# Kernel tuning notes

Hardware: AMD Instinct MI355X
Metric: run time of the kernel (lower is better)

Reference implementation:

```python
import jax, jax.numpy as jnp
import numpy as np

G, T, E, D, C = 4, 2048, 8, 1024, 2048
CAP_FACTORS = (0.25, 0.25, 0.125, 0.125, 0.0625, 0.0625, 0.0625, 0.0625)


def setup_inputs() -> dict:
    key = jax.random.key(0)
    k1, k2 = jax.random.split(key, 2)
    token_inputs = jax.random.normal(k1, (G, T, D), dtype=jnp.float32)
    # RouterWeights: Linear(dim -> num_experts), weight ~ N(0, 0.02), bias = 0
    W = jax.random.normal(k2, (E, D), dtype=jnp.float32) * 0.02
    b = jnp.zeros((E,), dtype=jnp.float32)
    return {"token_inputs": token_inputs, "W": W, "b": b,
            "num_experts": E, "expert_capacity": C}


def reference(token_inputs, W, b, num_experts, expert_capacity):
    # router logits [G, T, E] (jitter_noise = 0, no padding mask)
    logits = jnp.einsum('gtd,ed->gte', token_inputs, W) + b
    probs = jax.nn.softmax(logits, axis=-1)

    caps = [max(1, int(f * expert_capacity)) for f in CAP_FACTORS]
    tokens = token_inputs.shape[1]

    disp_parts, comb_parts = [], []
    for i, cap in enumerate(caps):  # fixed small loop over experts
        # each expert chooses its top-`cap` tokens
        gate, idx = jax.lax.top_k(probs[:, :, i], cap)        # [G, cap]
        onehot = jax.nn.one_hot(idx, tokens, dtype=jnp.int32)  # [G, cap, T]
        d = jnp.transpose(onehot, (0, 2, 1))                   # [G, T, cap]
        c = gate[:, None, :] * d.astype(probs.dtype)           # [G, T, cap]
        pad = expert_capacity - cap
        disp_parts.append(jnp.pad(d, ((0, 0), (0, 0), (0, pad))))
        comb_parts.append(jnp.pad(c, ((0, 0), (0, 0), (0, pad))))

    dispatch_mask = jnp.stack(disp_parts, axis=2)   # [G, T, E, C] int32
    combine_array = jnp.stack(comb_parts, axis=2)   # [G, T, E, C] float32

    router_z_loss = jnp.mean(jnp.square(jax.nn.log_softmax(logits, axis=-1)))
    return dispatch_mask, combine_array, router_z_loss
```

## Files before the change

### kernel.cpp

```cpp
#include <hip/hip_runtime.h>

#define GG 4
#define TT 2048
#define EE 8
#define DD 1024
#define CC 2048

static constexpr long long GTEC = (long long)GG * TT * EE * CC;

__global__ __launch_bounds__(256) void router_probs_kernel(
    const float* __restrict__ x, const float* __restrict__ W,
    const float* __restrict__ bias, float* __restrict__ probs,
    float* __restrict__ zloss)
{
    __shared__ float sW[EE * DD];
    __shared__ float zpart[4];
    for (int i = threadIdx.x; i < EE * DD; i += 256) sW[i] = W[i];
    __syncthreads();

    const int wave = threadIdx.x >> 6;
    const int lane = threadIdx.x & 63;
    const int token = blockIdx.x * 4 + wave;
    const float* xr = x + (long long)token * DD;

    float acc[EE];
#pragma unroll
    for (int e = 0; e < EE; ++e) acc[e] = 0.f;

#pragma unroll 4
    for (int k = lane; k < DD; k += 64) {
        float xv = xr[k];
#pragma unroll
        for (int e = 0; e < EE; ++e)
            acc[e] = fmaf(xv, sW[e * DD + k], acc[e]);
    }

#pragma unroll
    for (int off = 32; off > 0; off >>= 1) {
#pragma unroll
        for (int e = 0; e < EE; ++e)
            acc[e] += __shfl_xor(acc[e], off, 64);
    }

#pragma unroll
    for (int e = 0; e < EE; ++e) acc[e] += bias[e];

    float m = acc[0];
#pragma unroll
    for (int e = 1; e < EE; ++e) m = fmaxf(m, acc[e]);
    float s = 0.f;
#pragma unroll
    for (int e = 0; e < EE; ++e) s += expf(acc[e] - m);
    float lse = m + logf(s);

    if (lane < EE)
        probs[(long long)token * EE + lane] = expf(acc[lane] - lse);

    if (lane == 0) {
        float zs = 0.f;
#pragma unroll
        for (int e = 0; e < EE; ++e) {
            float d = acc[e] - lse;
            zs = fmaf(d, d, zs);
        }
        zpart[wave] = zs;
    }
    __syncthreads();
    if (threadIdx.x == 0) {
        float zb = (zpart[0] + zpart[1]) + (zpart[2] + zpart[3]);
        atomicAdd(zloss, zb * (1.0f / ((float)GG * TT * EE)));
    }
}

__global__ __launch_bounds__(1024) void topk_scatter_kernel(
    const float* __restrict__ probs, float* __restrict__ out)
{
    __shared__ unsigned long long keys[TT];
    const int g = blockIdx.x >> 3;
    const int e = blockIdx.x & 7;
    const int caps[EE] = {512, 512, 256, 256, 128, 128, 128, 128};
    const int cap = caps[e];

    for (int t = threadIdx.x; t < TT; t += 1024) {
        float p = probs[((long long)g * TT + t) * EE + e];
        unsigned int pb = __float_as_uint(p);
        keys[t] = ((unsigned long long)pb << 32) |
                  (unsigned long long)(0xFFFFFFFFu - (unsigned)t);
    }
    __syncthreads();

    for (int k = 2; k <= TT; k <<= 1) {
        for (int j = k >> 1; j > 0; j >>= 1) {
            for (int v = threadIdx.x; v < TT; v += 1024) {
                int ixj = v ^ j;
                if (ixj > v) {
                    bool desc = ((v & k) == 0);
                    unsigned long long a = keys[v];
                    unsigned long long b = keys[ixj];
                    bool sw = desc ? (a < b) : (a > b);
                    if (sw) { keys[v] = b; keys[ixj] = a; }
                }
            }
            __syncthreads();
        }
    }

    if (threadIdx.x < cap) {
        unsigned long long kk = keys[threadIdx.x];
        int t = (int)(0xFFFFFFFFu - (unsigned)(kk & 0xFFFFFFFFull));
        float gate = __uint_as_float((unsigned)(kk >> 32));
        long long base = (((long long)g * TT + t) * EE + e) * CC + threadIdx.x;
        out[base] = 1.0f;
        out[GTEC + base] = gate;
    }
}

extern "C" void kernel_launch(void* const* d_in, const int* in_sizes, int n_in,
                              void* d_out, int out_size, void* d_ws, size_t ws_size,
                              hipStream_t stream) {
    const float* x    = (const float*)d_in[0];
    const float* W    = (const float*)d_in[1];
    const float* bias = (const float*)d_in[2];
    float* out   = (float*)d_out;
    float* probs = (float*)d_ws;

    hipMemsetAsync(d_out, 0, (size_t)out_size * sizeof(float), stream);

    router_probs_kernel<<<GG * TT / 4, 256, 0, stream>>>(
        x, W, bias, probs, out + 2 * GTEC);

    topk_scatter_kernel<<<GG * EE, 1024, 0, stream>>>(probs, out);
}
```

Baseline: 1.089 ms.

## Fuse output zero-fill into router kernel and replace bitonic sort with rank counting

The hipMemset of the output is replaced by a zero-fill done by 7 of every 8 blocks of the router kernel, so the fill overlaps the router matmul. The single-block-per-(g,e) bitonic sort is replaced by a counting-rank kernel spread over 256 blocks, where each token computes its rank against all 2048 probabilities and scatters itself if the rank is below the expert's capacity. The z-loss atomic is replaced by per-block partial sums reduced in a dedicated final block. The O(T^2) compare count per expert is higher than the sort's, but the work is spread across many more blocks. Ties are broken by lower index, which matches top_k.

```diff
diff --git a/kernel.cpp b/kernel.cpp
--- a/kernel.cpp
+++ b/kernel.cpp
@@ -7,111 +7,128 @@
 #define CC 2048
 
 static constexpr long long GTEC = (long long)GG * TT * EE * CC;
+static constexpr long long FILL4 = 2 * GTEC / 4;
+#define NBLK 16384
+#define NFILL 14336
+#define WS_ZBLK 0
+#define WS_PROBS 2048
 
-__global__ __launch_bounds__(256) void router_probs_kernel(
+__global__ __launch_bounds__(256) void k1_fill_probs(
     const float* __restrict__ x, const float* __restrict__ W,
-    const float* __restrict__ bias, float* __restrict__ probs,
-    float* __restrict__ zloss)
+    const float* __restrict__ bias, float* __restrict__ ws,
+    float* __restrict__ out)
 {
-    __shared__ float sW[EE * DD];
-    __shared__ float zpart[4];
-    for (int i = threadIdx.x; i < EE * DD; i += 256) sW[i] = W[i];
-    __syncthreads();
+    const int b = blockIdx.x;
+    if ((b & 7) == 7) {
+        __shared__ float sW[EE * DD];
+        __shared__ float zpart[4];
+        for (int i = threadIdx.x; i < EE * DD; i += 256) sW[i] = W[i];
+        __syncthreads();
 
-    const int wave = threadIdx.x >> 6;
-    const int lane = threadIdx.x & 63;
-    const int token = blockIdx.x * 4 + wave;
-    const float* xr = x + (long long)token * DD;
+        const int pid  = b >> 3;
+        const int wave = threadIdx.x >> 6;
+        const int lane = threadIdx.x & 63;
+        const int token = pid * 4 + wave;
+        const float* xr = x + (long long)token * DD;
 
-    float acc[EE];
+        float acc[EE];
 #pragma unroll
-    for (int e = 0; e < EE; ++e) acc[e] = 0.f;
+        for (int e = 0; e < EE; ++e) acc[e] = 0.f;
+#pragma unroll 4
+        for (int k = lane; k < DD; k += 64) {
+            float xv = xr[k];
+#pragma unroll
+            for (int e = 0; e < EE; ++e)
+                acc[e] = fmaf(xv, sW[e * DD + k], acc[e]);
+        }
+#pragma unroll
+        for (int off = 32; off > 0; off >>= 1) {
+#pragma unroll
+            for (int e = 0; e < EE; ++e)
+                acc[e] += __shfl_xor(acc[e], off, 64);
+        }
+#pragma unroll
+        for (int e = 0; e < EE; ++e) acc[e] += bias[e];
 
-#pragma unroll 4
-    for (int k = lane; k < DD; k += 64) {
-        float xv = xr[k];
+        float m = acc[0];
 #pragma unroll
-        for (int e = 0; e < EE; ++e)
-            acc[e] = fmaf(xv, sW[e * DD + k], acc[e]);
-    }
+        for (int e = 1; e < EE; ++e) m = fmaxf(m, acc[e]);
+        float s = 0.f;
+#pragma unroll
+        for (int e = 0; e < EE; ++e) s += expf(acc[e] - m);
+        float lse = m + logf(s);
 
+        if (lane < EE)
+            ws[WS_PROBS + (long long)token * EE + lane] = expf(acc[lane] - lse);
+
+        if (lane == 0) {
+            float zs = 0.f;
 #pragma unroll
-    for (int off = 32; off > 0; off >>= 1) {
-#pragma unroll
-        for (int e = 0; e < EE; ++e)
-            acc[e] += __shfl_xor(acc[e], off, 64);
-    }
-
-#pragma unroll
-    for (int e = 0; e < EE; ++e) acc[e] += bias[e];
-
-    float m = acc[0];
-#pragma unroll
-    for (int e = 1; e < EE; ++e) m = fmaxf(m, acc[e]);
-    float s = 0.f;
-#pragma unroll
-    for (int e = 0; e < EE; ++e) s += expf(acc[e] - m);
-    float lse = m + logf(s);
-
-    if (lane < EE)
-        probs[(long long)token * EE + lane] = expf(acc[lane] - lse);
-
-    if (lane == 0) {
-        float zs = 0.f;
-#pragma unroll
-        for (int e = 0; e < EE; ++e) {
-            float d = acc[e] - lse;
-            zs = fmaf(d, d, zs);
+            for (int e = 0; e < EE; ++e) {
+                float d = acc[e] - lse;
+                zs = fmaf(d, d, zs);
+            }
+            zpart[wave] = zs;
         }
-        zpart[wave] = zs;
-    }
-    __syncthreads();
-    if (threadIdx.x == 0) {
-        float zb = (zpart[0] + zpart[1]) + (zpart[2] + zpart[3]);
-        atomicAdd(zloss, zb * (1.0f / ((float)GG * TT * EE)));
+        __syncthreads();
+        if (threadIdx.x == 0)
+            ws[WS_ZBLK + pid] = (zpart[0] + zpart[1]) + (zpart[2] + zpart[3]);
+    } else {
+        const int fid = b - ((b + 1) >> 3);
+        float4* o4 = (float4*)out;
+        const float4 z = make_float4(0.f, 0.f, 0.f, 0.f);
+        for (long long i = (long long)fid * 256 + threadIdx.x; i < FILL4;
+             i += (long long)NFILL * 256)
+            o4[i] = z;
     }
 }
 
-__global__ __launch_bounds__(1024) void topk_scatter_kernel(
-    const float* __restrict__ probs, float* __restrict__ out)
+__global__ __launch_bounds__(256) void k2_rank_scatter(
+    const float* __restrict__ ws, float* __restrict__ out)
 {
-    __shared__ unsigned long long keys[TT];
-    const int g = blockIdx.x >> 3;
-    const int e = blockIdx.x & 7;
-    const int caps[EE] = {512, 512, 256, 256, 128, 128, 128, 128};
-    const int cap = caps[e];
+    __shared__ float sp[TT];
+    const int b = blockIdx.x;
+    if (b < 256) {
+        const int g = b >> 6;
+        const int e = (b >> 3) & 7;
+        const int chunk = b & 7;
+        const int caps[EE] = {512, 512, 256, 256, 128, 128, 128, 128};
+        const int cap = caps[e];
 
-    for (int t = threadIdx.x; t < TT; t += 1024) {
-        float p = probs[((long long)g * TT + t) * EE + e];
-        unsigned int pb = __float_as_uint(p);
-        keys[t] = ((unsigned long long)pb << 32) |
-                  (unsigned long long)(0xFFFFFFFFu - (unsigned)t);
-    }
-    __syncthreads();
+        for (int i = threadIdx.x; i < TT; i += 256)
+            sp[i] = ws[WS_PROBS + ((long long)g * TT + i) * EE + e];
+        __syncthreads();
 
-    for (int k = 2; k <= TT; k <<= 1) {
-        for (int j = k >> 1; j > 0; j >>= 1) {
-            for (int v = threadIdx.x; v < TT; v += 1024) {
-                int ixj = v ^ j;
-                if (ixj > v) {
-                    bool desc = ((v & k) == 0);
-                    unsigned long long a = keys[v];
-                    unsigned long long b = keys[ixj];
-                    bool sw = desc ? (a < b) : (a > b);
-                    if (sw) { keys[v] = b; keys[ixj] = a; }
-                }
-            }
-            __syncthreads();
+        const int t = chunk * 256 + threadIdx.x;
+        const float p = sp[t];
+        int rank = 0;
+        const float4* sp4 = (const float4*)sp;
+#pragma unroll 4
+        for (int j4 = 0; j4 < TT / 4; ++j4) {
+            float4 v = sp4[j4];
+            int j = j4 * 4;
+            rank += (v.x > p) || (v.x == p && (j + 0) < t);
+            rank += (v.y > p) || (v.y == p && (j + 1) < t);
+            rank += (v.z > p) || (v.z == p && (j + 2) < t);
+            rank += (v.w > p) || (v.w == p && (j + 3) < t);
         }
-    }
-
-    if (threadIdx.x < cap) {
-        unsigned long long kk = keys[threadIdx.x];
-        int t = (int)(0xFFFFFFFFu - (unsigned)(kk & 0xFFFFFFFFull));
-        float gate = __uint_as_float((unsigned)(kk >> 32));
-        long long base = (((long long)g * TT + t) * EE + e) * CC + threadIdx.x;
-        out[base] = 1.0f;
-        out[GTEC + base] = gate;
+        if (rank < cap) {
+            long long base = (((long long)g * TT + t) * EE + e) * CC + rank;
+            out[base] = 1.0f;
+            out[GTEC + base] = p;
+        }
+    } else {
+        float s = 0.f;
+        for (int i = threadIdx.x; i < 2048; i += 256)
+            s += ws[WS_ZBLK + i];
+#pragma unroll
+        for (int off = 32; off > 0; off >>= 1) s += __shfl_xor(s, off, 64);
+        __shared__ float red[4];
+        if ((threadIdx.x & 63) == 0) red[threadIdx.x >> 6] = s;
+        __syncthreads();
+        if (threadIdx.x == 0)
+            out[2 * GTEC] = ((red[0] + red[1]) + (red[2] + red[3])) *
+                            (1.0f / ((float)GG * TT * EE));
     }
 }
 
@@ -121,13 +138,9 @@
     const float* x    = (const float*)d_in[0];
     const float* W    = (const float*)d_in[1];
     const float* bias = (const float*)d_in[2];
-    float* out   = (float*)d_out;
-    float* probs = (float*)d_ws;
+    float* out = (float*)d_out;
+    float* ws  = (float*)d_ws;
 
-    hipMemsetAsync(d_out, 0, (size_t)out_size * sizeof(float), stream);
-
-    router_probs_kernel<<<GG * TT / 4, 256, 0, stream>>>(
-        x, W, bias, probs, out + 2 * GTEC);
-
-    topk_scatter_kernel<<<GG * EE, 1024, 0, stream>>>(probs, out);
+    k1_fill_probs<<<NBLK, 256, 0, stream>>>(x, W, bias, ws, out);
+    k2_rank_scatter<<<257, 256, 0, stream>>>(ws, out);
 }
```

Result: slower. 1.136 ms (+4.3%).
